# Performance work log

Measured on AMD Instinct MI355X. Metric: run time of the kernel, lower is better.

## Reference

```python
import jax, jax.numpy as jnp
import numpy as np

B, LRIS, HR = 2, 256, 1024
D, GH, GW = 8, 16, 16  # grid depth (lb) and grid spatial (lris/2^4)

PARAM_SHAPES = {
    'sw0': (8, 3, 3, 3),   'sb0': (8,),
    'sw1': (16, 8, 3, 3),  'sb1': (16,),
    'sw2': (32, 16, 3, 3), 'sb2': (32,),
    'sw3': (64, 32, 3, 3), 'sb3': (64,),
    'lw0': (64, 64, 3, 3), 'lb0': (64,),
    'lw1': (64, 64, 3, 3), 'lb1': (64,),
    'gcw0': (64, 64, 3, 3), 'gcb0': (64,),
    'gcw1': (64, 64, 3, 3), 'gcb1': (64,),
    'fcw0': (256, 1024),   'fcb0': (256,),
    'fcw1': (128, 256),    'fcb1': (128,),
    'fcw2': (64, 128),     'fcb2': (64,),
    'bgw': (96, 64, 1, 1), 'bgb': (96,),
    'guw0': (16, 3, 1, 1), 'gub0': (16,),
    'guw1': (1, 16, 1, 1), 'gub1': (1,),
}


def _conv(x, w, b, stride, pad, act):
    y = jax.lax.conv_general_dilated(x, w, (stride, stride), [(pad, pad), (pad, pad)],
                                     dimension_numbers=('NCHW', 'OIHW', 'NCHW'))
    y = y + b[None, :, None, None]
    if act == 'relu':
        y = jax.nn.relu(y)
    elif act == 'sigmoid':
        y = jax.nn.sigmoid(y)
    return y


def _slice_apply(grid, guide, fr):
    # grid: [B,12,D,GH,GW]; guide: [B,H,W] in [0,1]; fr: [B,3,H,W]
    Bq, C, Dq, gh, gw = grid.shape
    H, W = fr.shape[2], fr.shape[3]
    xs = (jnp.arange(W, dtype=jnp.float32) + 0.5) * gw / W - 0.5
    ys = (jnp.arange(H, dtype=jnp.float32) + 0.5) * gh / H - 0.5
    x0 = jnp.clip(jnp.floor(xs).astype(jnp.int32), 0, gw - 1); x1 = jnp.clip(x0 + 1, 0, gw - 1)
    y0 = jnp.clip(jnp.floor(ys).astype(jnp.int32), 0, gh - 1); y1 = jnp.clip(y0 + 1, 0, gh - 1)
    wx = xs - jnp.floor(xs)
    wy = ys - jnp.floor(ys)
    gz = guide * Dq - 0.5
    gridT = jnp.transpose(grid, (0, 2, 3, 4, 1))  # [B,D,GH,GW,C]

    def slice_one(g, gzb):
        z0 = jnp.clip(jnp.floor(gzb).astype(jnp.int32), 0, Dq - 1)
        z1 = jnp.clip(z0 + 1, 0, Dq - 1)
        wz = gzb - jnp.floor(gzb)  # [H,W]
        acc = jnp.zeros((H, W, C), dtype=g.dtype)
        for zi, wzf in ((z0, 1.0 - wz), (z1, wz)):
            for yi, wyf in ((y0, 1.0 - wy), (y1, wy)):
                for xi, wxf in ((x0, 1.0 - wx), (x1, wx)):
                    w = wzf * wyf[:, None] * wxf[None, :]
                    acc = acc + w[..., None] * g[zi, yi[:, None], xi[None, :]]
        return acc

    sliced = jax.vmap(slice_one)(gridT, gz)  # [B,H,W,12]
    A = sliced.reshape(Bq, H, W, 3, 4)       # per-pixel affine 3x4
    rgb = jnp.transpose(fr, (0, 2, 3, 1))    # [B,H,W,3]
    out = jnp.einsum('bhwoi,bhwi->bhwo', A[..., :3], rgb) + A[..., 3]
    return jnp.transpose(out, (0, 3, 1, 2))  # [B,3,H,W]


def _forward(lr, fr, p):
    x = _conv(lr, p['sw0'], p['sb0'], 2, 1, 'relu')
    x = _conv(x, p['sw1'], p['sb1'], 2, 1, 'relu')
    x = _conv(x, p['sw2'], p['sb2'], 2, 1, 'relu')
    x = _conv(x, p['sw3'], p['sb3'], 2, 1, 'relu')        # [B,64,16,16]
    loc = _conv(x, p['lw0'], p['lb0'], 1, 1, 'relu')
    loc = _conv(loc, p['lw1'], p['lb1'], 1, 1, None)      # [B,64,16,16]
    g = _conv(x, p['gcw0'], p['gcb0'], 2, 1, 'relu')
    g = _conv(g, p['gcw1'], p['gcb1'], 2, 1, 'relu')      # [B,64,4,4]
    g = g.reshape(g.shape[0], -1)                          # [B,1024]
    g = jax.nn.relu(g @ p['fcw0'].T + p['fcb0'])
    g = jax.nn.relu(g @ p['fcw1'].T + p['fcb1'])
    g = g @ p['fcw2'].T + p['fcb2']                        # [B,64]
    fus = jax.nn.relu(loc + g[:, :, None, None])           # Fusion: broadcast add + ReLU
    bg = _conv(fus, p['bgw'], p['bgb'], 1, 0, None)        # [B,96,16,16]
    grid = bg.reshape(bg.shape[0], 12, D, GH, GW)          # split(lb)+stack == reshape
    gd = _conv(fr, p['guw0'], p['gub0'], 1, 0, 'relu')
    gd = _conv(gd, p['guw1'], p['gub1'], 1, 0, 'sigmoid')[:, 0]  # [B,H,W]
    fin = _slice_apply(grid, gd, fr)
    return gd, fin


def setup_inputs() -> dict:
    key = jax.random.key(0)
    keys = jax.random.split(key, len(PARAM_SHAPES) + 2)
    inp = {}
    inp['lr'] = jax.random.uniform(keys[0], (B, 3, LRIS, LRIS), dtype=jnp.float32)
    inp['fr'] = jax.random.uniform(keys[1], (B, 3, HR, HR), dtype=jnp.float32)
    for i, (name, shp) in enumerate(PARAM_SHAPES.items()):
        inp[name] = jax.random.normal(keys[i + 2], shp, dtype=jnp.float32) * 0.05
    return inp


def reference(lr, fr, sw0, sb0, sw1, sb1, sw2, sb2, sw3, sb3, lw0, lb0, lw1, lb1,
              gcw0, gcb0, gcw1, gcb1, fcw0, fcb0, fcw1, fcb1, fcw2, fcb2,
              bgw, bgb, guw0, gub0, guw1, gub1):
    p = dict(sw0=sw0, sb0=sb0, sw1=sw1, sb1=sb1, sw2=sw2, sb2=sb2, sw3=sw3, sb3=sb3,
             lw0=lw0, lb0=lb0, lw1=lw1, lb1=lb1, gcw0=gcw0, gcb0=gcb0, gcw1=gcw1, gcb1=gcb1,
             fcw0=fcw0, fcb0=fcb0, fcw1=fcw1, fcb1=fcb1, fcw2=fcw2, fcb2=fcb2,
             bgw=bgw, bgb=bgb, guw0=guw0, gub0=gub0, guw1=guw1, gub1=gub1)
    return _forward(lr, fr, p)
```

## Files before the change

### kernel.cpp

```cpp
#include <hip/hip_runtime.h>
#include <math.h>

#define HW_ (1024*1024)

__device__ __forceinline__ float wave_red(float a) {
    a += __shfl_xor(a, 1);  a += __shfl_xor(a, 2);  a += __shfl_xor(a, 4);
    a += __shfl_xor(a, 8);  a += __shfl_xor(a, 16); a += __shfl_xor(a, 32);
    return a;
}

__global__ void k_splat(const float* __restrict__ lr,
                        const float* __restrict__ sw0, const float* __restrict__ sb0,
                        const float* __restrict__ sw1, const float* __restrict__ sb1,
                        const float* __restrict__ sw2, const float* __restrict__ sb2,
                        const float* __restrict__ sw3, const float* __restrict__ sb3,
                        float* __restrict__ ws3)
{
    __shared__ float lrs[3 * 31 * 32];
    __shared__ float s0b[8 * 15 * 16];
    __shared__ float s1b[16 * 7 * 8];
    __shared__ float s2b[32 * 9];
    __shared__ float w1s[1152];
    __shared__ float w2s[4608];
    int b = blockIdx.y;
    int ty = blockIdx.x >> 4, tx = blockIdx.x & 15;
    int t = threadIdx.x;

    for (int i = t; i < 2883; i += 256) {
        int c = i / 961, rem = i % 961, y = rem / 31, x = rem % 31;
        int gy = 16 * ty - 15 + y, gx = 16 * tx - 15 + x;
        float val = 0.f;
        if ((unsigned)gy < 256u && (unsigned)gx < 256u)
            val = lr[(((size_t)b * 3 + c) << 16) + (gy << 8) + gx];
        lrs[c * 992 + y * 32 + x] = val;
    }
    for (int i = t; i < 1152; i += 256) w1s[i] = sw1[i];
    for (int i = t; i < 4608; i += 256) w2s[i] = sw2[i];
    __syncthreads();

    for (int i = t; i < 1800; i += 256) {
        int c = i / 225, rem = i % 225, y = rem / 15, x = rem % 15;
        int gy = 8 * ty - 7 + y, gx = 8 * tx - 7 + x;
        float val = 0.f;
        if ((unsigned)gy < 128u && (unsigned)gx < 128u) {
            float acc = sb0[c];
            const float* wp = sw0 + c * 27;
            #pragma unroll
            for (int ci = 0; ci < 3; ci++) {
                const float* sp = lrs + ci * 992;
                #pragma unroll
                for (int kh = 0; kh < 3; kh++)
                    #pragma unroll
                    for (int kw = 0; kw < 3; kw++)
                        acc = fmaf(sp[(2 * y + kh) * 32 + 2 * x + kw],
                                   wp[ci * 9 + kh * 3 + kw], acc);
            }
            val = fmaxf(acc, 0.f);
        }
        s0b[c * 240 + y * 16 + x] = val;
    }
    __syncthreads();

    for (int i = t; i < 784; i += 256) {
        int c = i / 49, rem = i % 49, y = rem / 7, x = rem % 7;
        int gy = 4 * ty - 3 + y, gx = 4 * tx - 3 + x;
        float val = 0.f;
        if ((unsigned)gy < 64u && (unsigned)gx < 64u) {
            float acc = sb1[c];
            const float* wp = w1s + c * 72;
            #pragma unroll
            for (int ci = 0; ci < 8; ci++) {
                const float* sp = s0b + ci * 240;
                #pragma unroll
                for (int kh = 0; kh < 3; kh++)
                    #pragma unroll
                    for (int kw = 0; kw < 3; kw++)
                        acc = fmaf(sp[(2 * y + kh) * 16 + 2 * x + kw],
                                   wp[ci * 9 + kh * 3 + kw], acc);
            }
            val = fmaxf(acc, 0.f);
        }
        s1b[c * 56 + y * 8 + x] = val;
    }
    __syncthreads();

    for (int i = t; i < 288; i += 256) {
        int c = i / 9, rem = i % 9, y = rem / 3, x = rem % 3;
        int gy = 2 * ty - 1 + y, gx = 2 * tx - 1 + x;
        float val = 0.f;
        if ((unsigned)gy < 32u && (unsigned)gx < 32u) {
            float acc = sb2[c];
            const float* wp = w2s + c * 144;
            #pragma unroll
            for (int ci = 0; ci < 16; ci++) {
                const float* sp = s1b + ci * 56;
                #pragma unroll
                for (int kh = 0; kh < 3; kh++)
                    #pragma unroll
                    for (int kw = 0; kw < 3; kw++)
                        acc = fmaf(sp[(2 * y + kh) * 8 + 2 * x + kw],
                                   wp[ci * 9 + kh * 3 + kw], acc);
            }
            val = fmaxf(acc, 0.f);
        }
        s2b[c * 9 + y * 3 + x] = val;
    }
    __syncthreads();

    {
        int c = t >> 2, sub = t & 3;
        float acc = 0.f;
        const float* wp = sw3 + c * 288 + sub * 72;
        #pragma unroll
        for (int ci8 = 0; ci8 < 8; ci8++) {
            const float* sp = s2b + (sub * 8 + ci8) * 9;
            #pragma unroll
            for (int k = 0; k < 9; k++)
                acc = fmaf(sp[k], wp[ci8 * 9 + k], acc);
        }
        acc += __shfl_xor(acc, 1);
        acc += __shfl_xor(acc, 2);
        if (sub == 0)
            ws3[(((size_t)b * 64 + c) * 16 + ty) * 16 + tx] = fmaxf(acc + sb3[c], 0.f);
    }
}

__global__ void k_loc0_gc0(const float* __restrict__ ws3,
                           const float* __restrict__ lw0, const float* __restrict__ lb0,
                           float* __restrict__ loc0,
                           const float* __restrict__ gcw0, const float* __restrict__ gcb0,
                           float* __restrict__ g0)
{
    __shared__ float smem[20736];
    float* inp = smem;
    float* wgt = smem + 18432;
    int b = blockIdx.y, t = threadIdx.x;

    for (int i = t; i < 2048; i += 256) {
        int ci = i >> 5, rem = i & 31;
        inp[ci * 288 + (rem >> 1) * 18 + (rem & 1) * 17] = 0.f;
    }
    {
        const float4* src = (const float4*)(ws3 + ((size_t)b << 14));
        #pragma unroll
        for (int k = 0; k < 16; k++) {
            int i = t + (k << 8);
            float4 vv = src[i];
            int flat = i << 2;
            float* d = inp + (flat >> 8) * 288 + ((flat >> 4) & 15) * 18 + (flat & 15) + 1;
            d[0] = vv.x; d[1] = vv.y; d[2] = vv.z; d[3] = vv.w;
        }
    }
    if (blockIdx.x < 64) {
        int co = blockIdx.x;
        if (t < 144) ((float4*)wgt)[t] = ((const float4*)(lw0 + co * 576))[t];
        __syncthreads();
        int ho = t >> 4, wo = t & 15;
        float a0 = 0.f, a1 = 0.f, a2 = 0.f, a3 = 0.f;
        for (int ci = 0; ci < 16; ci++) {
            #pragma unroll
            for (int kh = 0; kh < 3; kh++) {
                int hi = ho - 1 + kh;
                if ((unsigned)hi >= 16u) continue;
                const float* qa = inp + ci * 288 + hi * 18 + wo;
                const float* wa = wgt + ci * 9 + kh * 3;
                a0 = fmaf(qa[0], wa[0], a0); a0 = fmaf(qa[1], wa[1], a0); a0 = fmaf(qa[2], wa[2], a0);
                const float* qb = qa + 16 * 288; const float* wb2 = wa + 144;
                a1 = fmaf(qb[0], wb2[0], a1); a1 = fmaf(qb[1], wb2[1], a1); a1 = fmaf(qb[2], wb2[2], a1);
                const float* qc = qa + 32 * 288; const float* wc = wa + 288;
                a2 = fmaf(qc[0], wc[0], a2); a2 = fmaf(qc[1], wc[1], a2); a2 = fmaf(qc[2], wc[2], a2);
                const float* qd = qa + 48 * 288; const float* wd = wa + 432;
                a3 = fmaf(qd[0], wd[0], a3); a3 = fmaf(qd[1], wd[1], a3); a3 = fmaf(qd[2], wd[2], a3);
            }
        }
        float acc = lb0[co] + ((a0 + a1) + (a2 + a3));
        loc0[((size_t)(b * 64 + co) << 8) + t] = fmaxf(acc, 0.f);
    } else {
        int cb = (blockIdx.x - 64) << 2;
        for (int i = t; i < 2304; i += 256) wgt[i] = gcw0[cb * 576 + i];
        __syncthreads();
        int sub = t >> 6, co = cb + sub;
        int px = t & 63, ho = px >> 3, wo = px & 7;
        const float* wb = wgt + sub * 576;
        float a0 = 0.f, a1 = 0.f, a2 = 0.f, a3 = 0.f;
        for (int ci = 0; ci < 16; ci++) {
            #pragma unroll
            for (int kh = 0; kh < 3; kh++) {
                int hi = (ho << 1) - 1 + kh;
                if ((unsigned)hi >= 16u) continue;
                const float* qa = inp + ci * 288 + hi * 18 + (wo << 1);
                const float* wa = wb + ci * 9 + kh * 3;
                a0 = fmaf(qa[0], wa[0], a0); a0 = fmaf(qa[1], wa[1], a0); a0 = fmaf(qa[2], wa[2], a0);
                const float* qb = qa + 16 * 288; const float* wb2 = wa + 144;
                a1 = fmaf(qb[0], wb2[0], a1); a1 = fmaf(qb[1], wb2[1], a1); a1 = fmaf(qb[2], wb2[2], a1);
                const float* qc = qa + 32 * 288; const float* wc = wa + 288;
                a2 = fmaf(qc[0], wc[0], a2); a2 = fmaf(qc[1], wc[1], a2); a2 = fmaf(qc[2], wc[2], a2);
                const float* qd = qa + 48 * 288; const float* wd = wa + 432;
                a3 = fmaf(qd[0], wd[0], a3); a3 = fmaf(qd[1], wd[1], a3); a3 = fmaf(qd[2], wd[2], a3);
            }
        }
        float acc = gcb0[co] + ((a0 + a1) + (a2 + a3));
        g0[((size_t)(b * 64 + co) << 6) + px] = fmaxf(acc, 0.f);
    }
}

__global__ void k_loc1_gc1(const float* __restrict__ loc0,
                           const float* __restrict__ lw1, const float* __restrict__ lb1,
                           float* __restrict__ loc,
                           const float* __restrict__ g0,
                           const float* __restrict__ gcw1, const float* __restrict__ gcb1,
                           float* __restrict__ v)
{
    __shared__ float smem[19008];
    int b = blockIdx.y, t = threadIdx.x;
    if (blockIdx.x < 64) {
        float* inp = smem;
        float* wloc = smem + 18432;
        int co = blockIdx.x;
        for (int i = t; i < 2048; i += 256) {
            int ci = i >> 5, rem = i & 31;
            inp[ci * 288 + (rem >> 1) * 18 + (rem & 1) * 17] = 0.f;
        }
        const float4* src = (const float4*)(loc0 + ((size_t)b << 14));
        #pragma unroll
        for (int k = 0; k < 16; k++) {
            int i = t + (k << 8);
            float4 vv = src[i];
            int flat = i << 2;
            float* d = inp + (flat >> 8) * 288 + ((flat >> 4) & 15) * 18 + (flat & 15) + 1;
            d[0] = vv.x; d[1] = vv.y; d[2] = vv.z; d[3] = vv.w;
        }
        if (t < 144) ((float4*)wloc)[t] = ((const float4*)(lw1 + co * 576))[t];
        __syncthreads();
        int ho = t >> 4, wo = t & 15;
        float a0 = 0.f, a1 = 0.f, a2 = 0.f, a3 = 0.f;
        for (int ci = 0; ci < 16; ci++) {
            #pragma unroll
            for (int kh = 0; kh < 3; kh++) {
                int hi = ho - 1 + kh;
                if ((unsigned)hi >= 16u) continue;
                const float* qa = inp + ci * 288 + hi * 18 + wo;
                const float* wa = wloc + ci * 9 + kh * 3;
                a0 = fmaf(qa[0], wa[0], a0); a0 = fmaf(qa[1], wa[1], a0); a0 = fmaf(qa[2], wa[2], a0);
                const float* qb = qa + 16 * 288; const float* wb2 = wa + 144;
                a1 = fmaf(qb[0], wb2[0], a1); a1 = fmaf(qb[1], wb2[1], a1); a1 = fmaf(qb[2], wb2[2], a1);
                const float* qc = qa + 32 * 288; const float* wc = wa + 288;
                a2 = fmaf(qc[0], wc[0], a2); a2 = fmaf(qc[1], wc[1], a2); a2 = fmaf(qc[2], wc[2], a2);
                const float* qd = qa + 48 * 288; const float* wd = wa + 432;
                a3 = fmaf(qd[0], wd[0], a3); a3 = fmaf(qd[1], wd[1], a3); a3 = fmaf(qd[2], wd[2], a3);
            }
        }
        loc[((size_t)(b * 64 + co) << 8) + t] = lb1[co] + ((a0 + a1) + (a2 + a3));
    } else {
        float* inp = smem;
        float* wgt = smem + 5120;
        int cb = (blockIdx.x - 64) << 4;
        for (int i = t; i < 1024; i += 256) {
            int ci = i >> 4, rem = i & 15;
            inp[ci * 80 + (rem >> 1) * 10 + (rem & 1) * 9] = 0.f;
        }
        const float4* src = (const float4*)(g0 + ((size_t)b << 12));
        #pragma unroll
        for (int k = 0; k < 4; k++) {
            int i = t + (k << 8);
            float4 vv = src[i];
            int flat = i << 2;
            float* d = inp + (flat >> 6) * 80 + ((flat >> 3) & 7) * 10 + (flat & 7) + 1;
            d[0] = vv.x; d[1] = vv.y; d[2] = vv.z; d[3] = vv.w;
        }
        for (int i = t; i < 9216; i += 256) wgt[i] = gcw1[cb * 576 + i];
        __syncthreads();
        int sub = t >> 4, co = cb + sub;
        int px = t & 15, ho = px >> 2, wo = px & 3;
        const float* wb = wgt + sub * 576;
        float a0 = 0.f, a1 = 0.f, a2 = 0.f, a3 = 0.f;
        for (int ci = 0; ci < 16; ci++) {
            #pragma unroll
            for (int kh = 0; kh < 3; kh++) {
                int hi = (ho << 1) - 1 + kh;
                if ((unsigned)hi >= 8u) continue;
                const float* qa = inp + ci * 80 + hi * 10 + (wo << 1);
                const float* wa = wb + ci * 9 + kh * 3;
                a0 = fmaf(qa[0], wa[0], a0); a0 = fmaf(qa[1], wa[1], a0); a0 = fmaf(qa[2], wa[2], a0);
                const float* qb = qa + 16 * 80; const float* wb2 = wa + 144;
                a1 = fmaf(qb[0], wb2[0], a1); a1 = fmaf(qb[1], wb2[1], a1); a1 = fmaf(qb[2], wb2[2], a1);
                const float* qc = qa + 32 * 80; const float* wc = wa + 288;
                a2 = fmaf(qc[0], wc[0], a2); a2 = fmaf(qc[1], wc[1], a2); a2 = fmaf(qc[2], wc[2], a2);
                const float* qd = qa + 48 * 80; const float* wd = wa + 432;
                a3 = fmaf(qd[0], wd[0], a3); a3 = fmaf(qd[1], wd[1], a3); a3 = fmaf(qd[2], wd[2], a3);
            }
        }
        float acc = gcb1[co] + ((a0 + a1) + (a2 + a3));
        v[((size_t)b << 10) + (co << 4) + px] = fmaxf(acc, 0.f);
    }
}

__global__ void k_fc0(const float* __restrict__ in, const float* __restrict__ w,
                      const float* __restrict__ bias, float* __restrict__ out)
{
    int gw = (blockIdx.x * blockDim.x + threadIdx.x) >> 6;
    int lane = threadIdx.x & 63;
    int b = gw >> 8, o = gw & 255;
    const float4* wr = (const float4*)(w + o * 1024);
    const float4* vr = (const float4*)(in + b * 1024);
    float acc = 0.f;
    #pragma unroll
    for (int i = 0; i < 4; i++) {
        float4 a = wr[i * 64 + lane];
        float4 x = vr[i * 64 + lane];
        acc += a.x * x.x + a.y * x.y + a.z * x.z + a.w * x.w;
    }
    acc = wave_red(acc);
    if (lane == 0) out[b * 256 + o] = fmaxf(acc + bias[o], 0.f);
}

__global__ void k_fc12bg(const float* __restrict__ h0,
                         const float* __restrict__ fcw1, const float* __restrict__ fcb1,
                         const float* __restrict__ fcw2, const float* __restrict__ fcb2,
                         const float* __restrict__ loc,
                         const float* __restrict__ bgw, const float* __restrict__ bgb,
                         float* __restrict__ grid_r)
{
    __shared__ float h0s[256];
    __shared__ float h1s[128];
    __shared__ float gvs[64];
    __shared__ float fus[1024];
    __shared__ float bgws[96 * 65];
    int b = blockIdx.y, r = blockIdx.x;
    int t = threadIdx.x, lane = t & 63, wv = t >> 6;

    h0s[t] = h0[b * 256 + t];
    for (int i = t; i < 6144; i += 256) bgws[(i >> 6) * 65 + (i & 63)] = bgw[i];
    __syncthreads();
    {
        float4 x4 = ((float4*)h0s)[lane];
        #pragma unroll 2
        for (int i = 0; i < 32; i++) {
            int o = (wv << 5) + i;
            float4 a = ((const float4*)(fcw1 + o * 256))[lane];
            float acc = a.x * x4.x + a.y * x4.y + a.z * x4.z + a.w * x4.w;
            acc = wave_red(acc);
            if (lane == 0) h1s[o] = fmaxf(acc + fcb1[o], 0.f);
        }
    }
    __syncthreads();
    {
        float2 x2 = ((float2*)h1s)[lane];
        #pragma unroll 2
        for (int i = 0; i < 16; i++) {
            int o = (wv << 4) + i;
            float2 a = ((const float2*)(fcw2 + o * 128))[lane];
            float acc = a.x * x2.x + a.y * x2.y;
            acc = wave_red(acc);
            if (lane == 0) gvs[o] = acc + fcb2[o];
        }
    }
    __syncthreads();
    #pragma unroll
    for (int i = 0; i < 4; i++) {
        int idx = t + (i << 8);
        int c = idx >> 4, p = idx & 15;
        fus[idx] = fmaxf(loc[(((size_t)b * 64 + c) * 16 + r) * 16 + p] + gvs[c], 0.f);
    }
    __syncthreads();
    {
        int p = t & 15, cg = t >> 4;
        float acc6[6];
        #pragma unroll
        for (int j = 0; j < 6; j++) acc6[j] = bgb[cg + (j << 4)];
        #pragma unroll 8
        for (int k = 0; k < 64; k++) {
            float f = fus[k * 16 + p];
            #pragma unroll
            for (int j = 0; j < 6; j++)
                acc6[j] += bgws[(cg + (j << 4)) * 65 + k] * f;
        }
        #pragma unroll
        for (int j = 0; j < 6; j++) {
            int co = cg + (j << 4);
            int c12 = co >> 3, d = co & 7;
            grid_r[(((((size_t)b * 8 + d) * 16 + r) * 16 + p) * 12) + c12] = acc6[j];
        }
    }
}

__global__ void guide_slice(const float* __restrict__ fr, const float* __restrict__ grid_r,
                            const float* __restrict__ guw0, const float* __restrict__ gub0,
                            const float* __restrict__ guw1, const float* __restrict__ gub1,
                            float* __restrict__ gd_out, float* __restrict__ fin_out)
{
    __shared__ float gy[8 * 196];
    int y = blockIdx.x, b = blockIdx.y;
    int t = threadIdx.x;

    float ys = (y + 0.5f) * 0.015625f - 0.5f;
    float fy = floorf(ys);
    int y0 = min(max((int)fy, 0), 15), y1 = min(y0 + 1, 15);
    float wy = ys - fy;

    const float* gb = grid_r + (size_t)b * 24576;
    for (int i = t; i < 1536; i += 256) {
        int z = i / 192, rem = i - z * 192;
        float a = gb[z * 3072 + y0 * 192 + rem];
        float c = gb[z * 3072 + y1 * 192 + rem];
        gy[z * 196 + rem] = a + wy * (c - a);
    }
    __syncthreads();

    int rowoff = (y << 10) + (t << 2);
    const float* frb = fr + (size_t)b * 3 * HW_;
    float4 R4 = *(const float4*)(frb + rowoff);
    float4 G4 = *(const float4*)(frb + HW_ + rowoff);
    float4 B4 = *(const float4*)(frb + 2 * HW_ + rowoff);
    float rr[4] = {R4.x, R4.y, R4.z, R4.w};
    float gg[4] = {G4.x, G4.y, G4.z, G4.w};
    float bb[4] = {B4.x, B4.y, B4.z, B4.w};
    float gdv[4], O0[4], O1[4], O2[4];

    #pragma unroll
    for (int j = 0; j < 4; j++) {
        float r = rr[j], g = gg[j], bl = bb[j];
        float s = gub1[0];
        #pragma unroll
        for (int c = 0; c < 16; c++) {
            float h = fmaf(guw0[c * 3], r, fmaf(guw0[c * 3 + 1], g,
                      fmaf(guw0[c * 3 + 2], bl, gub0[c])));
            s = fmaf(guw1[c], fmaxf(h, 0.f), s);
        }
        float gd = 1.f / (1.f + __expf(-s));
        gdv[j] = gd;

        int x = (t << 2) + j;
        float xs = (x + 0.5f) * 0.015625f - 0.5f;
        float fx = floorf(xs);
        int x0 = min(max((int)fx, 0), 15), x1 = min(x0 + 1, 15);
        float wx = xs - fx;
        float gz = gd * 8.f - 0.5f;
        float fz = floorf(gz);
        int z0 = min(max((int)fz, 0), 7), z1 = min(z0 + 1, 7);
        float wz = gz - fz;

        float acc[12];
        #pragma unroll
        for (int c = 0; c < 12; c++) acc[c] = 0.f;
        #pragma unroll
        for (int zi = 0; zi < 2; zi++) {
            int z = zi ? z1 : z0;
            float wzf = zi ? wz : 1.f - wz;
            const float4* p0 = (const float4*)(gy + z * 196 + x0 * 12);
            const float4* p1 = (const float4*)(gy + z * 196 + x1 * 12);
            float w0 = wzf * (1.f - wx), w1 = wzf * wx;
            #pragma unroll
            for (int q = 0; q < 3; q++) {
                float4 a = p0[q], c4 = p1[q];
                acc[q * 4 + 0] += w0 * a.x + w1 * c4.x;
                acc[q * 4 + 1] += w0 * a.y + w1 * c4.y;
                acc[q * 4 + 2] += w0 * a.z + w1 * c4.z;
                acc[q * 4 + 3] += w0 * a.w + w1 * c4.w;
            }
        }
        O0[j] = fmaf(acc[0], r, fmaf(acc[1], g, fmaf(acc[2], bl, acc[3])));
        O1[j] = fmaf(acc[4], r, fmaf(acc[5], g, fmaf(acc[6], bl, acc[7])));
        O2[j] = fmaf(acc[8], r, fmaf(acc[9], g, fmaf(acc[10], bl, acc[11])));
    }

    *(float4*)(gd_out + (size_t)b * HW_ + rowoff) = make_float4(gdv[0], gdv[1], gdv[2], gdv[3]);
    float* fb = fin_out + (size_t)b * 3 * HW_;
    *(float4*)(fb + rowoff)           = make_float4(O0[0], O0[1], O0[2], O0[3]);
    *(float4*)(fb + HW_ + rowoff)     = make_float4(O1[0], O1[1], O1[2], O1[3]);
    *(float4*)(fb + 2 * HW_ + rowoff) = make_float4(O2[0], O2[1], O2[2], O2[3]);
}

extern "C" void kernel_launch(void* const* d_in, const int* in_sizes, int n_in,
                              void* d_out, int out_size, void* d_ws, size_t ws_size,
                              hipStream_t stream) {
    const float* lr   = (const float*)d_in[0];
    const float* fr   = (const float*)d_in[1];
    const float* sw0  = (const float*)d_in[2];  const float* sb0 = (const float*)d_in[3];
    const float* sw1  = (const float*)d_in[4];  const float* sb1 = (const float*)d_in[5];
    const float* sw2  = (const float*)d_in[6];  const float* sb2 = (const float*)d_in[7];
    const float* sw3  = (const float*)d_in[8];  const float* sb3 = (const float*)d_in[9];
    const float* lw0  = (const float*)d_in[10]; const float* lb0 = (const float*)d_in[11];
    const float* lw1  = (const float*)d_in[12]; const float* lb1 = (const float*)d_in[13];
    const float* gcw0 = (const float*)d_in[14]; const float* gcb0 = (const float*)d_in[15];
    const float* gcw1 = (const float*)d_in[16]; const float* gcb1 = (const float*)d_in[17];
    const float* fcw0 = (const float*)d_in[18]; const float* fcb0 = (const float*)d_in[19];
    const float* fcw1 = (const float*)d_in[20]; const float* fcb1 = (const float*)d_in[21];
    const float* fcw2 = (const float*)d_in[22]; const float* fcb2 = (const float*)d_in[23];
    const float* bgw  = (const float*)d_in[24]; const float* bgb = (const float*)d_in[25];
    const float* guw0 = (const float*)d_in[26]; const float* gub0 = (const float*)d_in[27];
    const float* guw1 = (const float*)d_in[28]; const float* gub1 = (const float*)d_in[29];

    float* ws = (float*)d_ws;
    float* ws3    = ws;
    float* loc0   = ws + 32768;
    float* loc    = ws + 65536;
    float* g0     = ws + 98304;
    float* v      = ws + 106496;
    float* h0     = ws + 108544;
    float* grid_r = ws + 109056;

    float* gd_out  = (float*)d_out;
    float* fin_out = (float*)d_out + 2 * HW_;

    const int B = 2;

    k_splat<<<dim3(256, B), 256, 0, stream>>>(lr, sw0, sb0, sw1, sb1,
                                              sw2, sb2, sw3, sb3, ws3);
    k_loc0_gc0<<<dim3(80, B), 256, 0, stream>>>(ws3, lw0, lb0, loc0, gcw0, gcb0, g0);
    k_loc1_gc1<<<dim3(68, B), 256, 0, stream>>>(loc0, lw1, lb1, loc, g0, gcw1, gcb1, v);
    k_fc0<<<dim3(128), 256, 0, stream>>>(v, fcw0, fcb0, h0);
    k_fc12bg<<<dim3(16, B), 256, 0, stream>>>(h0, fcw1, fcb1, fcw2, fcb2,
                                              loc, bgw, bgb, grid_r);
    guide_slice<<<dim3(1024, B), 256, 0, stream>>>(
        fr, grid_r, guw0, gub0, guw1, gub1, gd_out, fin_out);
}
```

Measured before the change: 104.1 us.

## Fuse global conv gc1 with fc0 by recomputing gc1 per block

The separate fc0 kernel is removed and merged into the gc1 branch of the loc1 kernel. Each of 32 extra blocks per batch recomputes the full 64-channel gc1 output into shared memory, then computes 8 fc0 outputs from it. This drops one kernel launch and the global round trip of the v buffer, at the cost of redundant gc1 computation and weight loading in every block. The bgw shared-memory staging in fc12bg is also vectorised to float4 loads.

```diff
diff --git a/kernel.cpp b/kernel.cpp
--- a/kernel.cpp
+++ b/kernel.cpp
@@ -204,12 +204,13 @@
     }
 }
 
-__global__ void k_loc1_gc1(const float* __restrict__ loc0,
-                           const float* __restrict__ lw1, const float* __restrict__ lb1,
-                           float* __restrict__ loc,
-                           const float* __restrict__ g0,
-                           const float* __restrict__ gcw1, const float* __restrict__ gcb1,
-                           float* __restrict__ v)
+__global__ void k_loc1_fc(const float* __restrict__ loc0,
+                          const float* __restrict__ lw1, const float* __restrict__ lb1,
+                          float* __restrict__ loc,
+                          const float* __restrict__ g0,
+                          const float* __restrict__ gcw1, const float* __restrict__ gcb1,
+                          const float* __restrict__ fcw0, const float* __restrict__ fcb0,
+                          float* __restrict__ h0)
 {
     __shared__ float smem[19008];
     int b = blockIdx.y, t = threadIdx.x;
@@ -253,8 +254,9 @@
         loc[((size_t)(b * 64 + co) << 8) + t] = lb1[co] + ((a0 + a1) + (a2 + a3));
     } else {
         float* inp = smem;
-        float* wgt = smem + 5120;
-        int cb = (blockIdx.x - 64) << 4;
+        float* vls = smem + 5120;
+        float* wgt = smem + 6144;
+        int j = blockIdx.x - 64;
         for (int i = t; i < 1024; i += 256) {
             int ci = i >> 4, rem = i & 15;
             inp[ci * 80 + (rem >> 1) * 10 + (rem & 1) * 9] = 0.f;
@@ -268,50 +270,49 @@
             float* d = inp + (flat >> 6) * 80 + ((flat >> 3) & 7) * 10 + (flat & 7) + 1;
             d[0] = vv.x; d[1] = vv.y; d[2] = vv.z; d[3] = vv.w;
         }
-        for (int i = t; i < 9216; i += 256) wgt[i] = gcw1[cb * 576 + i];
+        int sub = t >> 4, px = t & 15, ho = px >> 2, wo = px & 3;
+        for (int cc = 0; cc < 4; cc++) {
+            __syncthreads();
+            for (int i = t; i < 9216; i += 256) wgt[i] = gcw1[cc * 9216 + i];
+            __syncthreads();
+            int co = (cc << 4) + sub;
+            const float* wb = wgt + sub * 576;
+            float a0 = 0.f, a1 = 0.f, a2 = 0.f, a3 = 0.f;
+            for (int ci = 0; ci < 16; ci++) {
+                #pragma unroll
+                for (int kh = 0; kh < 3; kh++) {
+                    int hi = (ho << 1) - 1 + kh;
+                    if ((unsigned)hi >= 8u) continue;
+                    const float* qa = inp + ci * 80 + hi * 10 + (wo << 1);
+                    const float* wa = wb + ci * 9 + kh * 3;
+                    a0 = fmaf(qa[0], wa[0], a0); a0 = fmaf(qa[1], wa[1], a0); a0 = fmaf(qa[2], wa[2], a0);
+                    const float* qb = qa + 16 * 80; const float* wb2 = wa + 144;
+                    a1 = fmaf(qb[0], wb2[0], a1); a1 = fmaf(qb[1], wb2[1], a1); a1 = fmaf(qb[2], wb2[2], a1);
+                    const float* qc = qa + 32 * 80; const float* wc = wa + 288;
+                    a2 = fmaf(qc[0], wc[0], a2); a2 = fmaf(qc[1], wc[1], a2); a2 = fmaf(qc[2], wc[2], a2);
+                    const float* qd = qa + 48 * 80; const float* wd = wa + 432;
+                    a3 = fmaf(qd[0], wd[0], a3); a3 = fmaf(qd[1], wd[1], a3); a3 = fmaf(qd[2], wd[2], a3);
+                }
+            }
+            vls[(co << 4) + px] = fmaxf(gcb1[co] + ((a0 + a1) + (a2 + a3)), 0.f);
+        }
         __syncthreads();
-        int sub = t >> 4, co = cb + sub;
-        int px = t & 15, ho = px >> 2, wo = px & 3;
-        const float* wb = wgt + sub * 576;
-        float a0 = 0.f, a1 = 0.f, a2 = 0.f, a3 = 0.f;
-        for (int ci = 0; ci < 16; ci++) {
-            #pragma unroll
-            for (int kh = 0; kh < 3; kh++) {
-                int hi = (ho << 1) - 1 + kh;
-                if ((unsigned)hi >= 8u) continue;
-                const float* qa = inp + ci * 80 + hi * 10 + (wo << 1);
-                const float* wa = wb + ci * 9 + kh * 3;
-                a0 = fmaf(qa[0], wa[0], a0); a0 = fmaf(qa[1], wa[1], a0); a0 = fmaf(qa[2], wa[2], a0);
-                const float* qb = qa + 16 * 80; const float* wb2 = wa + 144;
-                a1 = fmaf(qb[0], wb2[0], a1); a1 = fmaf(qb[1], wb2[1], a1); a1 = fmaf(qb[2], wb2[2], a1);
-                const float* qc = qa + 32 * 80; const float* wc = wa + 288;
-                a2 = fmaf(qc[0], wc[0], a2); a2 = fmaf(qc[1], wc[1], a2); a2 = fmaf(qc[2], wc[2], a2);
-                const float* qd = qa + 48 * 80; const float* wd = wa + 432;
-                a3 = fmaf(qd[0], wd[0], a3); a3 = fmaf(qd[1], wd[1], a3); a3 = fmaf(qd[2], wd[2], a3);
-            }
-        }
-        float acc = gcb1[co] + ((a0 + a1) + (a2 + a3));
-        v[((size_t)b << 10) + (co << 4) + px] = fmaxf(acc, 0.f);
-    }
-}
-
-__global__ void k_fc0(const float* __restrict__ in, const float* __restrict__ w,
-                      const float* __restrict__ bias, float* __restrict__ out)
-{
-    int gw = (blockIdx.x * blockDim.x + threadIdx.x) >> 6;
-    int lane = threadIdx.x & 63;
-    int b = gw >> 8, o = gw & 255;
-    const float4* wr = (const float4*)(w + o * 1024);
-    const float4* vr = (const float4*)(in + b * 1024);
-    float acc = 0.f;
-    #pragma unroll
-    for (int i = 0; i < 4; i++) {
-        float4 a = wr[i * 64 + lane];
-        float4 x = vr[i * 64 + lane];
-        acc += a.x * x.x + a.y * x.y + a.z * x.z + a.w * x.w;
-    }
-    acc = wave_red(acc);
-    if (lane == 0) out[b * 256 + o] = fmaxf(acc + bias[o], 0.f);
+        int lane = t & 63, wv = t >> 6;
+        #pragma unroll
+        for (int k = 0; k < 2; k++) {
+            int o = (j << 3) + (wv << 1) + k;
+            const float4* wr = (const float4*)(fcw0 + o * 1024);
+            float acc = 0.f;
+            #pragma unroll
+            for (int i = 0; i < 4; i++) {
+                float4 aa = wr[i * 64 + lane];
+                float4 xx = ((float4*)vls)[i * 64 + lane];
+                acc += aa.x * xx.x + aa.y * xx.y + aa.z * xx.z + aa.w * xx.w;
+            }
+            acc = wave_red(acc);
+            if (lane == 0) h0[b * 256 + o] = fmaxf(acc + fcb0[o], 0.f);
+        }
+    }
 }
 
 __global__ void k_fc12bg(const float* __restrict__ h0,
@@ -330,7 +331,12 @@
     int t = threadIdx.x, lane = t & 63, wv = t >> 6;
 
     h0s[t] = h0[b * 256 + t];
-    for (int i = t; i < 6144; i += 256) bgws[(i >> 6) * 65 + (i & 63)] = bgw[i];
+    for (int i4 = t; i4 < 1536; i4 += 256) {
+        float4 vv = ((const float4*)bgw)[i4];
+        int row = i4 >> 4, col = (i4 & 15) << 2;
+        float* d = &bgws[row * 65 + col];
+        d[0] = vv.x; d[1] = vv.y; d[2] = vv.z; d[3] = vv.w;
+    }
     __syncthreads();
     {
         float4 x4 = ((float4*)h0s)[lane];
@@ -496,9 +502,8 @@
     float* loc0   = ws + 32768;
     float* loc    = ws + 65536;
     float* g0     = ws + 98304;
-    float* v      = ws + 106496;
-    float* h0     = ws + 108544;
-    float* grid_r = ws + 109056;
+    float* h0     = ws + 106496;
+    float* grid_r = ws + 107008;
 
     float* gd_out  = (float*)d_out;
     float* fin_out = (float*)d_out + 2 * HW_;
@@ -508,8 +513,8 @@
     k_splat<<<dim3(256, B), 256, 0, stream>>>(lr, sw0, sb0, sw1, sb1,
                                               sw2, sb2, sw3, sb3, ws3);
     k_loc0_gc0<<<dim3(80, B), 256, 0, stream>>>(ws3, lw0, lb0, loc0, gcw0, gcb0, g0);
-    k_loc1_gc1<<<dim3(68, B), 256, 0, stream>>>(loc0, lw1, lb1, loc, g0, gcw1, gcb1, v);
-    k_fc0<<<dim3(128), 256, 0, stream>>>(v, fcw0, fcb0, h0);
+    k_loc1_fc<<<dim3(96, B), 256, 0, stream>>>(loc0, lw1, lb1, loc, g0, gcw1, gcb1,
+                                               fcw0, fcb0, h0);
     k_fc12bg<<<dim3(16, B), 256, 0, stream>>>(h0, fcw1, fcb1, fcw2, fcb2,
                                               loc, bgw, bgb, grid_r);
     guide_slice<<<dim3(1024, B), 256, 0, stream>>>(
```

Measured after the change: 125.5 us. 20.6% more time.
